# Optimization experiments

Hardware: AMD Instinct MI355X
Metric: run time of the kernel (lower is better)

Reference implementation:

```python
import jax, jax.numpy as jnp
import numpy as np

B, H, W, IN_C = 2, 64, 64, 3
D = 192            # embed_dim
DEPTH = 4
DI = 2 * D         # d_inner (mamba expand=2)
DS = 16            # d_state
DC = 4             # d_conv
DTR = -(-D // 16)  # dt_rank = ceil(D/16) = 12
EPS = 1e-5


def setup_inputs() -> dict:
    key = jax.random.key(0)
    ks = jax.random.split(key, 8)
    def rn(k, shape, s=0.02):
        return jax.random.normal(k, shape, dtype=jnp.float32) * s
    x = jax.random.normal(ks[0], (B, IN_C, H, W), dtype=jnp.float32)
    proj_w = rn(ks[1], (D, IN_C))
    proj_b = jnp.zeros((D,), jnp.float32)
    lp_w = rn(ks[2], (DEPTH, D, 2 * D))          # linear_proj: (out=D, in=2D)
    lp_b = jnp.zeros((DEPTH, D), jnp.float32)
    norm_w = jnp.ones((DEPTH, D), jnp.float32)
    in_w = rn(ks[3], (DEPTH, 2 * DI, D))         # mamba in_proj (no bias)
    conv_w = rn(ks[4], (DEPTH, DI, DC), 0.1)     # depthwise causal conv1d
    conv_b = jnp.zeros((DEPTH, DI), jnp.float32)
    xproj_w = rn(ks[5], (DEPTH, DTR + 2 * DS, DI))
    dt_w = rn(ks[6], (DEPTH, DI, DTR), 0.1)
    dt0 = np.random.default_rng(0).uniform(1e-3, 0.1, size=(DEPTH, DI)).astype(np.float32)
    dt_b = jnp.asarray(np.log(np.expm1(dt0)))    # softplus-inverse init (mamba default)
    A_log = jnp.tile(jnp.log(jnp.arange(1, DS + 1, dtype=jnp.float32)), (DEPTH, DI, 1))
    Dp = jnp.ones((DEPTH, DI), jnp.float32)
    out_w = rn(ks[7], (DEPTH, D, DI))
    normf_w = jnp.ones((D,), jnp.float32)
    return dict(x=x, proj_w=proj_w, proj_b=proj_b, lp_w=lp_w, lp_b=lp_b,
                norm_w=norm_w, in_w=in_w, conv_w=conv_w, conv_b=conv_b,
                xproj_w=xproj_w, dt_w=dt_w, dt_b=dt_b, A_log=A_log, Dp=Dp,
                out_w=out_w, normf_w=normf_w)


def _rmsnorm(x, w):
    return x * jax.lax.rsqrt(jnp.mean(x * x, axis=-1, keepdims=True) + EPS) * w


def _mamba(x, in_w, conv_w, conv_b, xproj_w, dt_w, dt_b, A_log, Dp, out_w):
    # x: (B, N, D)
    Bsz = x.shape[0]
    xz = jnp.einsum('bnd,ed->bne', x, in_w)                 # (B,N,2*DI)
    xi, z = jnp.split(xz, 2, axis=-1)
    # causal depthwise conv1d along sequence (pad left d_conv-1)
    xt = xi.transpose(0, 2, 1)                              # (B,DI,N)
    xc = jax.lax.conv_general_dilated(xt, conv_w[:, None, :], (1,), [(DC - 1, 0)],
                                      feature_group_count=DI)
    xi = jax.nn.silu((xc + conv_b[None, :, None]).transpose(0, 2, 1))  # (B,N,DI)
    dbc = jnp.einsum('bni,ei->bne', xi, xproj_w)            # (B,N,DTR+2*DS)
    dt = jax.nn.softplus(jnp.einsum('bnr,ir->bni', dbc[..., :DTR], dt_w) + dt_b)
    Bm = dbc[..., DTR:DTR + DS]                             # (B,N,DS)
    Cm = dbc[..., DTR + DS:]                                # (B,N,DS)
    A = -jnp.exp(A_log)                                     # (DI,DS)
    dA = jnp.exp(dt[..., None] * A)                         # (B,N,DI,DS)
    dBx = dt[..., None] * Bm[:, :, None, :] * xi[..., None] # (B,N,DI,DS)
    def step(h, inp):
        a, bx = inp
        h = a * h + bx
        return h, h
    h0 = jnp.zeros((Bsz, DI, DS), x.dtype)
    _, hs = jax.lax.scan(step, h0, (dA.transpose(1, 0, 2, 3), dBx.transpose(1, 0, 2, 3)))
    y = jnp.einsum('nbis,bns->bni', hs, Cm) + Dp * xi
    y = y * jax.nn.silu(z)
    return jnp.einsum('bni,di->bnd', y, out_w)


def _block(x, lp_w, lp_b, norm_w, mp):
    # DeltaVisionMambaBlock: token-diff -> linear_proj -> RMSNorm -> Mamba -> +skip
    prev = jnp.concatenate([jnp.zeros_like(x[:, :1]), x[:, :-1]], axis=1)
    comb = jnp.concatenate([x, x - prev], axis=-1)          # (B,N,2D)
    proj = jnp.einsum('bnc,dc->bnd', comb, lp_w) + lp_b
    return _mamba(_rmsnorm(proj, norm_w), *mp) + x


def reference(x, proj_w, proj_b, lp_w, lp_b, norm_w, in_w, conv_w, conv_b,
              xproj_w, dt_w, dt_b, A_log, Dp, out_w, normf_w):
    Bsz = x.shape[0]
    feat = jnp.einsum('bchw,dc->bdhw', x, proj_w) + proj_b[None, :, None, None]
    seq = feat.reshape(Bsz, D, H * W).transpose(0, 2, 1)    # (B,N,D)
    for l in range(DEPTH):
        mp = (in_w[l], conv_w[l], conv_b[l], xproj_w[l], dt_w[l], dt_b[l],
              A_log[l], Dp[l], out_w[l])
        seq = _block(seq, lp_w[l], lp_b[l], norm_w[l], mp)
    seq = _rmsnorm(seq, normf_w)
    return seq.transpose(0, 2, 1).reshape(Bsz, D, H, W)
```

## Files before the change

kernel.cpp:

```cpp
#include <hip/hip_runtime.h>
#include <hip/hip_bf16.h>

#define BB 2
#define NN 4096
#define DD 192
#define DI 384
#define DS 16
#define DTR 12
#define DC 4
#define DEPTH 4
#define NT (BB*NN)
#define NCH 128
#define CL 32
#define EPSF 1e-5f

#define OFF_X       0
#define OFF_PROJ_W  24576
#define OFF_PROJ_B  25152
#define OFF_LP_W    25344
#define OFF_LP_B    320256
#define OFF_NORM_W  321024
#define OFF_IN_W    321792
#define OFF_CONV_W  911616
#define OFF_CONV_B  917760
#define OFF_XPROJ_W 919296
#define OFF_DT_W    986880
#define OFF_DT_B    1005312
#define OFF_A_LOG   1006848
#define OFF_DP      1031424
#define OFF_OUT_W   1032960
#define OFF_NORMF_W 1327872
#define ARENA_TOTAL 1328064
#define ARENA_BYTES 2656160

typedef __hip_bfloat16 bf16_t;
typedef unsigned short u16;
typedef unsigned int u32;
typedef __attribute__((ext_vector_type(8))) unsigned short u16x8;
typedef __attribute__((ext_vector_type(8))) short s16x8;
typedef __attribute__((ext_vector_type(4))) float f32x4;

struct Ptrs { const void* p[16]; };

__device__ __forceinline__ float bf(u16 v){ return __uint_as_float(((u32)v)<<16); }
__device__ __forceinline__ u16 f2bf(float f){
  u32 b = __float_as_uint(f);
  return (u16)((b + 0x7FFFu + ((b>>16)&1u)) >> 16);
}

__global__ __launch_bounds__(256) void k_detect(const u16* __restrict__ x, int* flag){
  __shared__ int cnt;
  if (threadIdx.x==0) cnt=0;
  __syncthreads();
  u32 v = x[2*threadIdx.x];
  int ex = (int)((v>>7)&0xFF);
  if (ex>=100 && ex<=140) atomicAdd(&cnt,1);
  __syncthreads();
  if (threadIdx.x==0) *flag = (cnt>128) ? 0 : 1;
}

__global__ __launch_bounds__(256) void k_cvt(Ptrs ps, const int* __restrict__ flag, u16* __restrict__ arena){
  int e = blockIdx.x*256 + threadIdx.x;
  if (e >= ARENA_TOTAL) return;
  const void* sp; int off;
  if      (e < OFF_PROJ_W ){ sp=ps.p[0];  off=OFF_X; }
  else if (e < OFF_PROJ_B ){ sp=ps.p[1];  off=OFF_PROJ_W; }
  else if (e < OFF_LP_W   ){ sp=ps.p[2];  off=OFF_PROJ_B; }
  else if (e < OFF_LP_B   ){ sp=ps.p[3];  off=OFF_LP_W; }
  else if (e < OFF_NORM_W ){ sp=ps.p[4];  off=OFF_LP_B; }
  else if (e < OFF_IN_W   ){ sp=ps.p[5];  off=OFF_NORM_W; }
  else if (e < OFF_CONV_W ){ sp=ps.p[6];  off=OFF_IN_W; }
  else if (e < OFF_CONV_B ){ sp=ps.p[7];  off=OFF_CONV_W; }
  else if (e < OFF_XPROJ_W){ sp=ps.p[8];  off=OFF_CONV_B; }
  else if (e < OFF_DT_W   ){ sp=ps.p[9];  off=OFF_XPROJ_W; }
  else if (e < OFF_DT_B   ){ sp=ps.p[10]; off=OFF_DT_W; }
  else if (e < OFF_A_LOG  ){ sp=ps.p[11]; off=OFF_DT_B; }
  else if (e < OFF_DP     ){ sp=ps.p[12]; off=OFF_A_LOG; }
  else if (e < OFF_OUT_W  ){ sp=ps.p[13]; off=OFF_DP; }
  else if (e < OFF_NORMF_W){ sp=ps.p[14]; off=OFF_OUT_W; }
  else                     { sp=ps.p[15]; off=OFF_NORMF_W; }
  int k = e - off;
  if (*flag){
    u32 v = ((const u32*)sp)[k];
    arena[e] = (u16)((v + 0x7FFFu + ((v>>16)&1u)) >> 16);
  } else {
    arena[e] = ((const u16*)sp)[k];
  }
}

__global__ __launch_bounds__(256) void k_proj(const u16* __restrict__ x, const u16* __restrict__ pw,
                                              const u16* __restrict__ pb, float* __restrict__ seq){
  int idx = blockIdx.x*256 + threadIdx.x;
  if (idx >= NT*DD) return;
  int d = idx % DD; int bn = idx / DD; int b = bn >> 12; int n = bn & (NN-1);
  float acc = bf(pb[d]);
  acc += bf(x[(b*3+0)*NN + n]) * bf(pw[d*3+0]);
  acc += bf(x[(b*3+1)*NN + n]) * bf(pw[d*3+1]);
  acc += bf(x[(b*3+2)*NN + n]) * bf(pw[d*3+2]);
  seq[idx] = acc;
}

__global__ __launch_bounds__(256) void k_lp_norm(const float* __restrict__ seq,
    const u16* __restrict__ lp_w, const u16* __restrict__ lp_b, const u16* __restrict__ norm_w,
    u16* __restrict__ xn){
  const int tid = threadIdx.x;
  const int n0 = blockIdx.x*32;
  __shared__ u16 combL[32][392];
  __shared__ u16 wL[192][136];
  __shared__ float accL[32][200];
  __shared__ float ssq[32];

  for (int idx = tid*4; idx < 32*DD; idx += 1024){
    int t = idx/DD, d = idx%DD;
    int gn = n0 + t;
    float4 cur = *(const float4*)&seq[gn*DD + d];
    float4 prv = make_float4(0.f,0.f,0.f,0.f);
    if ((gn & (NN-1)) != 0) prv = *(const float4*)&seq[(gn-1)*DD + d];
    combL[t][d+0]=f2bf(cur.x); combL[t][d+1]=f2bf(cur.y); combL[t][d+2]=f2bf(cur.z); combL[t][d+3]=f2bf(cur.w);
    combL[t][DD+d+0]=f2bf(cur.x-prv.x); combL[t][DD+d+1]=f2bf(cur.y-prv.y);
    combL[t][DD+d+2]=f2bf(cur.z-prv.z); combL[t][DD+d+3]=f2bf(cur.w-prv.w);
  }

  const int w = tid >> 6;
  const int lane = tid & 63;
  const int lm = lane & 15, lk = lane >> 4;
  const int mt = w & 1;
  const int nbase = (w >> 1)*6;

  f32x4 acc[6];
  #pragma unroll
  for (int i=0;i<6;++i) acc[i] = (f32x4){0.f,0.f,0.f,0.f};

  for (int c=0;c<3;++c){
    const int kc = c*128;
    for (int idx = tid*8; idx < 192*128; idx += 2048){
      int row = idx >> 7, col = idx & 127;
      *(u16x8*)&wL[row][col] = *(const u16x8*)(lp_w + row*384 + kc + col);
    }
    __syncthreads();
    #pragma unroll
    for (int ks=0; ks<4; ++ks){
      s16x8 a = *(s16x8*)&combL[mt*16 + lm][kc + ks*32 + lk*8];
      #pragma unroll
      for (int nt=0; nt<6; ++nt){
        s16x8 b = *(s16x8*)&wL[(nbase+nt)*16 + lm][ks*32 + lk*8];
        acc[nt] = __builtin_amdgcn_mfma_f32_16x16x32_bf16(a, b, acc[nt], 0, 0, 0);
      }
    }
    __syncthreads();
  }
  #pragma unroll
  for (int nt=0; nt<6; ++nt){
    #pragma unroll
    for (int r=0; r<4; ++r){
      int m = mt*16 + lk*4 + r;
      int n = (nbase+nt)*16 + lm;
      accL[m][n] = acc[nt][r] + bf(lp_b[n]);
    }
  }
  __syncthreads();
  {
    int tok = tid >> 3, j = tid & 7;
    float s = 0.f;
    #pragma unroll
    for (int c=0;c<24;++c){ float v = accL[tok][j*24+c]; s += v*v; }
    s += __shfl_xor(s,1); s += __shfl_xor(s,2); s += __shfl_xor(s,4);
    if (j==0) ssq[tok] = rsqrtf(s*(1.f/DD) + EPSF);
  }
  __syncthreads();
  for (int idx = tid; idx < 32*DD; idx += 256){
    int t = idx/DD, d = idx%DD;
    xn[(n0+t)*DD + d] = f2bf(accL[t][d] * ssq[t] * bf(norm_w[d]));
  }
}

__global__ __launch_bounds__(256) void k_inproj(const u16* __restrict__ xn,
    const u16* __restrict__ in_w, u16* __restrict__ xi_c, u16* __restrict__ zz_b){
  const int tid = threadIdx.x;
  const int m0 = blockIdx.x*64;
  const int e0 = blockIdx.y*64;
  __shared__ u16 aL[64][200];
  __shared__ u16 bL[64][200];
  for (int idx = tid*8; idx < 64*192; idx += 2048){
    int row = idx/192, col = idx%192;
    *(u16x8*)&aL[row][col] = *(const u16x8*)(xn   + (m0+row)*192 + col);
    *(u16x8*)&bL[row][col] = *(const u16x8*)(in_w + (e0+row)*192 + col);
  }
  __syncthreads();
  const int w = tid >> 6, lane = tid & 63;
  const int lm = lane & 15, lk = lane >> 4;
  f32x4 acc[4];
  #pragma unroll
  for (int i=0;i<4;++i) acc[i] = (f32x4){0.f,0.f,0.f,0.f};
  #pragma unroll
  for (int ks=0; ks<6; ++ks){
    s16x8 a = *(s16x8*)&aL[w*16 + lm][ks*32 + lk*8];
    #pragma unroll
    for (int nt=0; nt<4; ++nt){
      s16x8 b = *(s16x8*)&bL[nt*16 + lm][ks*32 + lk*8];
      acc[nt] = __builtin_amdgcn_mfma_f32_16x16x32_bf16(a, b, acc[nt], 0, 0, 0);
    }
  }
  #pragma unroll
  for (int nt=0; nt<4; ++nt){
    int e = e0 + nt*16 + lm;
    #pragma unroll
    for (int r=0; r<4; ++r){
      int tok = m0 + w*16 + lk*4 + r;
      u16 v = f2bf(acc[nt][r]);
      if (e0 < DI) xi_c[tok*DI + e]      = v;
      else         zz_b[tok*DI + e - DI] = v;
    }
  }
}

__global__ __launch_bounds__(256) void k_conv(const u16* __restrict__ xi_c,
    const u16* __restrict__ conv_w, const u16* __restrict__ conv_b,
    u16* __restrict__ xc_b, float* __restrict__ xi){
  int idx = blockIdx.x*256 + threadIdx.x;
  int i = idx % DI; int bg = idx / DI;
  int nstart = bg*4;
  int base = nstart & ~(NN-1);
  float w0 = bf(conv_w[i*4+0]), w1 = bf(conv_w[i*4+1]), w2 = bf(conv_w[i*4+2]), w3 = bf(conv_w[i*4+3]);
  float cb = bf(conv_b[i]);
  float xv[7];
  #pragma unroll
  for (int t=0; t<3; ++t){
    int bn2 = nstart - 3 + t;
    xv[t] = (bn2 >= base) ? bf(xi_c[bn2*DI + i]) : 0.f;
  }
  #pragma unroll
  for (int t=3; t<7; ++t) xv[t] = bf(xi_c[(nstart + t - 3)*DI + i]);
  #pragma unroll
  for (int t=0; t<4; ++t){
    float acc = cb + xv[t]*w0 + xv[t+1]*w1 + xv[t+2]*w2 + xv[t+3]*w3;
    float v = acc/(1.f+__expf(-acc));
    int o = (nstart+t)*DI + i;
    xc_b[o] = f2bf(v);
    xi[o] = v;
  }
}

__global__ __launch_bounds__(256) void k_xproj_dt(const u16* __restrict__ xc,
    const u16* __restrict__ xproj_w, const u16* __restrict__ dt_w, const u16* __restrict__ dt_bv,
    float* __restrict__ dt_o, float* __restrict__ Bm, float* __restrict__ Cm){
  const int tid = threadIdx.x;
  const int n0 = blockIdx.x*32;
  __shared__ u16 xcL[32][392];
  __shared__ u16 dtwL[384][24];
  __shared__ float dbcL[32][16];
  for (int idx=tid; idx<512; idx+=256) ((float*)dbcL)[idx]=0.f;
  for (int idx=tid*8; idx<32*384; idx+=2048){
    int r=idx/384, c=idx%384;
    *(u16x8*)&xcL[r][c] = *(const u16x8*)(xc + (n0+r)*DI + c);
  }
  for (int idx=tid; idx<384*12; idx+=256){
    int r=idx/12, c=idx%12;
    dtwL[r][c] = dt_w[idx];
    dtwL[r][12+c] = 0;
  }
  __syncthreads();
  const int w = tid>>6, lane = tid&63, lm = lane&15, lk = lane>>4;
  const int mt = w & 1, nh = w >> 1;
  const s16x8 zb = {0,0,0,0,0,0,0,0};
  if (nh == 0){
    f32x4 acc0 = {0.f,0.f,0.f,0.f}, acc1 = {0.f,0.f,0.f,0.f};
    #pragma unroll
    for (int ks=0; ks<12; ++ks){
      s16x8 a = *(s16x8*)&xcL[mt*16+lm][ks*32+lk*8];
      s16x8 b0 = *(const s16x8*)(xproj_w + lm*384 + ks*32 + lk*8);
      s16x8 b1 = *(const s16x8*)(xproj_w + (16+lm)*384 + ks*32 + lk*8);
      acc0 = __builtin_amdgcn_mfma_f32_16x16x32_bf16(a, b0, acc0, 0, 0, 0);
      acc1 = __builtin_amdgcn_mfma_f32_16x16x32_bf16(a, b1, acc1, 0, 0, 0);
    }
    #pragma unroll
    for (int r=0;r<4;++r){
      int m = mt*16 + lk*4 + r;
      int gm = n0 + m;
      if (lm < 12) dbcL[m][lm] = acc0[r];
      else         Bm[gm*DS + lm-12] = acc0[r];
      int e1 = 16+lm;
      if (e1 < 28) Bm[gm*DS + e1-12] = acc1[r];
      else         Cm[gm*DS + e1-28] = acc1[r];
    }
  } else {
    f32x4 acc2 = {0.f,0.f,0.f,0.f};
    #pragma unroll
    for (int ks=0; ks<12; ++ks){
      s16x8 a = *(s16x8*)&xcL[mt*16+lm][ks*32+lk*8];
      s16x8 b2 = (lm<12) ? *(const s16x8*)(xproj_w + (32+lm)*384 + ks*32 + lk*8) : zb;
      acc2 = __builtin_amdgcn_mfma_f32_16x16x32_bf16(a, b2, acc2, 0, 0, 0);
    }
    #pragma unroll
    for (int r=0;r<4;++r){
      int m = mt*16 + lk*4 + r;
      int e2 = 32+lm;
      if (e2 < 44) Cm[(n0+m)*DS + e2-28] = acc2[r];
    }
  }
  __syncthreads();
  s16x8 a_dt = zb;
  if (lk < 2){
    #pragma unroll
    for (int j=0;j<8;++j) a_dt[j] = (short)f2bf(dbcL[mt*16+lm][lk*8+j]);
  }
  #pragma unroll
  for (int q=0;q<12;++q){
    int nt = nh*12 + q;
    s16x8 b = (lk<2) ? *(s16x8*)&dtwL[nt*16+lm][lk*8] : zb;
    f32x4 acc = {0.f,0.f,0.f,0.f};
    acc = __builtin_amdgcn_mfma_f32_16x16x32_bf16(a_dt, b, acc, 0, 0, 0);
    int i = nt*16 + lm;
    float bias = bf(dt_bv[i]);
    #pragma unroll
    for (int r=0;r<4;++r){
      int m = mt*16 + lk*4 + r;
      float xval = acc[r] + bias;
      float sp = (xval>20.f)? xval : log1pf(__expf(xval));
      dt_o[(n0+m)*DI + i] = sp;
    }
  }
}

__global__ __launch_bounds__(128) void k_scan1(const float* __restrict__ dt,
    const float* __restrict__ xi, const float* __restrict__ Bm,
    const u16* __restrict__ A_log, float* __restrict__ P, float* __restrict__ Q){
  const int tid = threadIdx.x;
  const int i = blockIdx.x*128 + tid;
  const int ch = blockIdx.y, b = blockIdx.z;
  __shared__ float bm_l[CL][DS];
  {
    int r = tid>>2, c4 = (tid&3)*4;
    *(float4*)&bm_l[r][c4] = *(const float4*)&Bm[(b*NN + ch*CL + r)*DS + c4];
  }
  float Av[DS];
  {
    u16x8 a0 = *(const u16x8*)(A_log + i*DS);
    u16x8 a1 = *(const u16x8*)(A_log + i*DS + 8);
    #pragma unroll
    for (int s=0;s<8;++s){ Av[s] = -__expf(bf(a0[s])); Av[8+s] = -__expf(bf(a1[s])); }
  }
  __syncthreads();
  float Pv[DS], h[DS];
  #pragma unroll
  for (int s=0;s<DS;++s){ Pv[s]=1.f; h[s]=0.f; }
  const int nb = b*NN + ch*CL;
  #pragma unroll 4
  for (int t=0;t<CL;++t){
    float dtv = dt[(nb+t)*DI + i];
    float xv  = xi[(nb+t)*DI + i];
    float dtx = dtv*xv;
    #pragma unroll
    for (int s=0;s<DS;++s){
      float a = __expf(dtv*Av[s]);
      Pv[s] *= a;
      h[s] = a*h[s] + dtx*bm_l[t][s];
    }
  }
  const int base = ((b*DI + i)*NCH + ch)*DS;
  #pragma unroll
  for (int s4=0;s4<4;++s4){
    *(float4*)&P[base+s4*4] = make_float4(Pv[s4*4+0],Pv[s4*4+1],Pv[s4*4+2],Pv[s4*4+3]);
    *(float4*)&Q[base+s4*4] = make_float4(h[s4*4+0],h[s4*4+1],h[s4*4+2],h[s4*4+3]);
  }
}

__global__ __launch_bounds__(256) void k_scan2(const float* __restrict__ P, const float* __restrict__ Q,
                                               float* __restrict__ Hin){
  int tid = blockIdx.x*256 + threadIdx.x;
  int s = tid & 15; int ci = tid >> 4;
  float h = 0.f;
  for (int ch=0; ch<NCH; ++ch){
    int idx = (ci*NCH+ch)*DS + s;
    Hin[idx] = h;
    h = P[idx]*h + Q[idx];
  }
}

__global__ __launch_bounds__(128) void k_scan3(const float* __restrict__ dt,
    const float* __restrict__ xi, const float* __restrict__ Bm, const float* __restrict__ Cm,
    const u16* __restrict__ zz_b, const u16* __restrict__ A_log, const u16* __restrict__ Dp,
    const float* __restrict__ Hin, u16* __restrict__ Y){
  const int tid = threadIdx.x;
  const int i = blockIdx.x*128 + tid;
  const int ch = blockIdx.y, b = blockIdx.z;
  __shared__ float bm_l[CL][DS], cm_l[CL][DS];
  {
    int r = tid>>2, c4 = (tid&3)*4;
    *(float4*)&bm_l[r][c4] = *(const float4*)&Bm[(b*NN + ch*CL + r)*DS + c4];
    *(float4*)&cm_l[r][c4] = *(const float4*)&Cm[(b*NN + ch*CL + r)*DS + c4];
  }
  float Av[DS];
  {
    u16x8 a0 = *(const u16x8*)(A_log + i*DS);
    u16x8 a1 = *(const u16x8*)(A_log + i*DS + 8);
    #pragma unroll
    for (int s=0;s<8;++s){ Av[s] = -__expf(bf(a0[s])); Av[8+s] = -__expf(bf(a1[s])); }
  }
  const float Dv = bf(Dp[i]);
  float h[DS];
  const int base = ((b*DI + i)*NCH + ch)*DS;
  #pragma unroll
  for (int s4=0;s4<4;++s4){
    float4 hv = *(const float4*)&Hin[base+s4*4];
    h[s4*4+0]=hv.x; h[s4*4+1]=hv.y; h[s4*4+2]=hv.z; h[s4*4+3]=hv.w;
  }
  __syncthreads();
  const int nb = b*NN + ch*CL;
  #pragma unroll 4
  for (int t=0;t<CL;++t){
    float dtv = dt[(nb+t)*DI + i];
    float xv  = xi[(nb+t)*DI + i];
    float zv  = bf(zz_b[(nb+t)*DI + i]);
    float dtx = dtv*xv;
    float y = 0.f;
    #pragma unroll
    for (int s=0;s<DS;++s){
      float a = __expf(dtv*Av[s]);
      h[s] = a*h[s] + dtx*bm_l[t][s];
      y += h[s]*cm_l[t][s];
    }
    y += Dv*xv;
    y *= zv/(1.f+__expf(-zv));
    Y[(nb+t)*DI + i] = f2bf(y);
  }
}

__global__ __launch_bounds__(256) void k_out(const u16* __restrict__ Y,
    const u16* __restrict__ out_w, float* __restrict__ seq){
  const int tid = threadIdx.x;
  const int m0 = blockIdx.x*64;
  const int d0 = blockIdx.y*64;
  __shared__ u16 aL[64][200];
  __shared__ u16 bL[64][200];
  const int w = tid >> 6, lane = tid & 63;
  const int lm = lane & 15, lk = lane >> 4;
  f32x4 acc[4];
  #pragma unroll
  for (int i=0;i<4;++i) acc[i] = (f32x4){0.f,0.f,0.f,0.f};
  for (int c=0; c<2; ++c){
    const int kc = c*192;
    for (int idx = tid*8; idx < 64*192; idx += 2048){
      int row = idx/192, col = idx%192;
      *(u16x8*)&aL[row][col] = *(const u16x8*)(Y     + (m0+row)*DI + kc + col);
      *(u16x8*)&bL[row][col] = *(const u16x8*)(out_w + (d0+row)*DI + kc + col);
    }
    __syncthreads();
    #pragma unroll
    for (int ks=0; ks<6; ++ks){
      s16x8 a = *(s16x8*)&aL[w*16 + lm][ks*32 + lk*8];
      #pragma unroll
      for (int nt=0; nt<4; ++nt){
        s16x8 b = *(s16x8*)&bL[nt*16 + lm][ks*32 + lk*8];
        acc[nt] = __builtin_amdgcn_mfma_f32_16x16x32_bf16(a, b, acc[nt], 0, 0, 0);
      }
    }
    __syncthreads();
  }
  #pragma unroll
  for (int nt=0; nt<4; ++nt){
    int d = d0 + nt*16 + lm;
    #pragma unroll
    for (int r=0; r<4; ++r){
      int tok = m0 + w*16 + lk*4 + r;
      seq[tok*DD + d] += acc[nt][r];
    }
  }
}

__global__ __launch_bounds__(192) void k_final(const float* __restrict__ seq,
    const u16* __restrict__ normf_w, void* __restrict__ out, const int* __restrict__ flag){
  const int d = threadIdx.x;
  const int bn = blockIdx.x;
  const int b = bn >> 12, n = bn & (NN-1);
  __shared__ float wred[3];
  float v = seq[bn*DD + d];
  float s = v*v;
  #pragma unroll
  for (int off=32; off>=1; off>>=1) s += __shfl_down(s,off);
  if ((d&63)==0) wred[d>>6]=s;
  __syncthreads();
  float r = rsqrtf((wred[0]+wred[1]+wred[2])*(1.f/DD) + EPSF);
  float res = v * r * bf(normf_w[d]);
  int o = (b*DD+d)*NN + n;
  if (*flag) ((float*)out)[o] = res;
  else       ((u16*)out)[o]   = f2bf(res);
}

extern "C" void kernel_launch(void* const* d_in, const int* in_sizes, int n_in,
                              void* d_out, int out_size, void* d_ws, size_t ws_size,
                              hipStream_t stream){
  Ptrs ps;
  for (int i=0;i<16;++i) ps.p[i] = d_in[i];

  u16* arena = (u16*)d_ws;
  int* flag  = (int*)(arena + ARENA_TOTAL);
  float* fbase = (float*)((char*)d_ws + ARENA_BYTES);

  float* seq  = fbase;
  float* xi   = seq  + NT*DD;
  float* dt   = xi   + NT*DI;
  float* Bm   = dt   + NT*DI;
  float* Cm   = Bm   + NT*DS;
  float* Hin  = Cm   + NT*DS;
  u16* xn_b   = (u16*)(Hin + BB*DI*NCH*DS);
  u16* xi_c   = xn_b + NT*DD;
  u16* zz_b   = xi_c + NT*DI;
  u16* Y_b    = zz_b + NT*DI;
  u16*   xc_b = Y_b;
  float* Pb   = (float*)Y_b;
  float* Qb   = (float*)xi_c;

  const u16* xA      = arena + OFF_X;
  const u16* proj_w  = arena + OFF_PROJ_W;
  const u16* proj_b  = arena + OFF_PROJ_B;
  const u16* lp_w    = arena + OFF_LP_W;
  const u16* lp_b    = arena + OFF_LP_B;
  const u16* norm_w  = arena + OFF_NORM_W;
  const u16* in_w    = arena + OFF_IN_W;
  const u16* conv_w  = arena + OFF_CONV_W;
  const u16* conv_b  = arena + OFF_CONV_B;
  const u16* xproj_w = arena + OFF_XPROJ_W;
  const u16* dt_w    = arena + OFF_DT_W;
  const u16* dt_b    = arena + OFF_DT_B;
  const u16* A_log   = arena + OFF_A_LOG;
  const u16* Dp      = arena + OFF_DP;
  const u16* out_w   = arena + OFF_OUT_W;
  const u16* normf_w = arena + OFF_NORMF_W;

  k_detect<<<1, 256, 0, stream>>>((const u16*)d_in[0], flag);
  k_cvt<<<(ARENA_TOTAL+255)/256, 256, 0, stream>>>(ps, flag, arena);

  k_proj<<<(NT*DD+255)/256, 256, 0, stream>>>(xA, proj_w, proj_b, seq);
  for (int l=0; l<DEPTH; ++l){
    k_lp_norm<<<NT/32, 256, 0, stream>>>(seq, lp_w + l*DD*2*DD, lp_b + l*DD, norm_w + l*DD, xn_b);
    k_inproj<<<dim3(NT/64, 12), 256, 0, stream>>>(xn_b, in_w + l*2*DI*DD, xi_c, zz_b);
    k_conv<<<(NT/4)*DI/256, 256, 0, stream>>>(xi_c, conv_w + l*DI*DC, conv_b + l*DI, xc_b, xi);
    k_xproj_dt<<<NT/32, 256, 0, stream>>>(xc_b, xproj_w + l*(DTR+2*DS)*DI, dt_w + l*DI*DTR,
        dt_b + l*DI, dt, Bm, Cm);
    k_scan1<<<dim3(DI/128, NCH, BB), 128, 0, stream>>>(dt, xi, Bm, A_log + l*DI*DS, Pb, Qb);
    k_scan2<<<(BB*DI*DS)/256, 256, 0, stream>>>(Pb, Qb, Hin);
    k_scan3<<<dim3(DI/128, NCH, BB), 128, 0, stream>>>(dt, xi, Bm, Cm, zz_b, A_log + l*DI*DS, Dp + l*DI, Hin, Y_b);
    k_out<<<dim3(NT/64, 3), 256, 0, stream>>>(Y_b, out_w + l*DD*DI, seq);
  }
  k_final<<<NT, 192, 0, stream>>>(seq, normf_w, d_out, flag);
}
```

Baseline: 613.1 us.

## Fuse linear_proj+norm with in_proj and recompute causal conv inside consumers

Merges the linear_proj/RMSNorm kernel with the in_proj GEMM, so the normalized activations stay in LDS instead of going through global memory. Removes the standalone conv kernel: xproj_dt and both scan kernels now recompute the depthwise causal conv plus SiLU from the bf16 in_proj output. This drops the fp32 xi buffer and two launches per layer. In exchange the conv and SiLU work is done three times, and in_proj weights are read straight from global memory with a 32-token tile per block, which lowers reuse and parallelism.

```diff
diff --git a/kernel.cpp b/kernel.cpp
--- a/kernel.cpp
+++ b/kernel.cpp
@@ -100,14 +100,15 @@
   seq[idx] = acc;
 }
 
-__global__ __launch_bounds__(256) void k_lp_norm(const float* __restrict__ seq,
+__global__ __launch_bounds__(256) void k_lp_in(const float* __restrict__ seq,
     const u16* __restrict__ lp_w, const u16* __restrict__ lp_b, const u16* __restrict__ norm_w,
-    u16* __restrict__ xn){
+    const u16* __restrict__ in_w, u16* __restrict__ xi_c, u16* __restrict__ zz_b){
   const int tid = threadIdx.x;
   const int n0 = blockIdx.x*32;
   __shared__ u16 combL[32][392];
   __shared__ u16 wL[192][136];
   __shared__ float accL[32][200];
+  __shared__ u16 xnL[32][200];
   __shared__ float ssq[32];
 
   for (int idx = tid*4; idx < 32*DD; idx += 1024){
@@ -124,38 +125,39 @@
   const int w = tid >> 6;
   const int lane = tid & 63;
   const int lm = lane & 15, lk = lane >> 4;
-  const int mt = w & 1;
-  const int nbase = (w >> 1)*6;
-
-  f32x4 acc[6];
-  #pragma unroll
-  for (int i=0;i<6;++i) acc[i] = (f32x4){0.f,0.f,0.f,0.f};
-
-  for (int c=0;c<3;++c){
-    const int kc = c*128;
-    for (int idx = tid*8; idx < 192*128; idx += 2048){
-      int row = idx >> 7, col = idx & 127;
-      *(u16x8*)&wL[row][col] = *(const u16x8*)(lp_w + row*384 + kc + col);
-    }
-    __syncthreads();
-    #pragma unroll
-    for (int ks=0; ks<4; ++ks){
-      s16x8 a = *(s16x8*)&combL[mt*16 + lm][kc + ks*32 + lk*8];
+
+  {
+    const int mt = w & 1;
+    const int nbase = (w >> 1)*6;
+    f32x4 acc[6];
+    #pragma unroll
+    for (int i=0;i<6;++i) acc[i] = (f32x4){0.f,0.f,0.f,0.f};
+    for (int c=0;c<3;++c){
+      const int kc = c*128;
+      for (int idx = tid*8; idx < 192*128; idx += 2048){
+        int row = idx >> 7, col = idx & 127;
+        *(u16x8*)&wL[row][col] = *(const u16x8*)(lp_w + row*384 + kc + col);
+      }
+      __syncthreads();
       #pragma unroll
-      for (int nt=0; nt<6; ++nt){
-        s16x8 b = *(s16x8*)&wL[(nbase+nt)*16 + lm][ks*32 + lk*8];
-        acc[nt] = __builtin_amdgcn_mfma_f32_16x16x32_bf16(a, b, acc[nt], 0, 0, 0);
-      }
-    }
-    __syncthreads();
-  }
-  #pragma unroll
-  for (int nt=0; nt<6; ++nt){
-    #pragma unroll
-    for (int r=0; r<4; ++r){
-      int m = mt*16 + lk*4 + r;
-      int n = (nbase+nt)*16 + lm;
-      accL[m][n] = acc[nt][r] + bf(lp_b[n]);
+      for (int ks=0; ks<4; ++ks){
+        s16x8 a = *(s16x8*)&combL[mt*16 + lm][kc + ks*32 + lk*8];
+        #pragma unroll
+        for (int nt=0; nt<6; ++nt){
+          s16x8 b = *(s16x8*)&wL[(nbase+nt)*16 + lm][ks*32 + lk*8];
+          acc[nt] = __builtin_amdgcn_mfma_f32_16x16x32_bf16(a, b, acc[nt], 0, 0, 0);
+        }
+      }
+      __syncthreads();
+    }
+    #pragma unroll
+    for (int nt=0; nt<6; ++nt){
+      #pragma unroll
+      for (int r=0; r<4; ++r){
+        int m = mt*16 + lk*4 + r;
+        int n = (nbase+nt)*16 + lm;
+        accL[m][n] = acc[nt][r] + bf(lp_b[n]);
+      }
     }
   }
   __syncthreads();
@@ -170,89 +172,88 @@
   __syncthreads();
   for (int idx = tid; idx < 32*DD; idx += 256){
     int t = idx/DD, d = idx%DD;
-    xn[(n0+t)*DD + d] = f2bf(accL[t][d] * ssq[t] * bf(norm_w[d]));
-  }
-}
-
-__global__ __launch_bounds__(256) void k_inproj(const u16* __restrict__ xn,
-    const u16* __restrict__ in_w, u16* __restrict__ xi_c, u16* __restrict__ zz_b){
-  const int tid = threadIdx.x;
-  const int m0 = blockIdx.x*64;
-  const int e0 = blockIdx.y*64;
-  __shared__ u16 aL[64][200];
-  __shared__ u16 bL[64][200];
-  for (int idx = tid*8; idx < 64*192; idx += 2048){
-    int row = idx/192, col = idx%192;
-    *(u16x8*)&aL[row][col] = *(const u16x8*)(xn   + (m0+row)*192 + col);
-    *(u16x8*)&bL[row][col] = *(const u16x8*)(in_w + (e0+row)*192 + col);
-  }
-  __syncthreads();
-  const int w = tid >> 6, lane = tid & 63;
-  const int lm = lane & 15, lk = lane >> 4;
-  f32x4 acc[4];
-  #pragma unroll
-  for (int i=0;i<4;++i) acc[i] = (f32x4){0.f,0.f,0.f,0.f};
-  #pragma unroll
-  for (int ks=0; ks<6; ++ks){
-    s16x8 a = *(s16x8*)&aL[w*16 + lm][ks*32 + lk*8];
-    #pragma unroll
-    for (int nt=0; nt<4; ++nt){
-      s16x8 b = *(s16x8*)&bL[nt*16 + lm][ks*32 + lk*8];
-      acc[nt] = __builtin_amdgcn_mfma_f32_16x16x32_bf16(a, b, acc[nt], 0, 0, 0);
-    }
-  }
-  #pragma unroll
-  for (int nt=0; nt<4; ++nt){
-    int e = e0 + nt*16 + lm;
-    #pragma unroll
-    for (int r=0; r<4; ++r){
-      int tok = m0 + w*16 + lk*4 + r;
-      u16 v = f2bf(acc[nt][r]);
-      if (e0 < DI) xi_c[tok*DI + e]      = v;
-      else         zz_b[tok*DI + e - DI] = v;
-    }
-  }
-}
-
-__global__ __launch_bounds__(256) void k_conv(const u16* __restrict__ xi_c,
+    xnL[t][d] = f2bf(accL[t][d] * ssq[t] * bf(norm_w[d]));
+  }
+  __syncthreads();
+  {
+    f32x4 acc2[12][2];
+    #pragma unroll
+    for (int nt=0; nt<12; ++nt){
+      acc2[nt][0] = (f32x4){0.f,0.f,0.f,0.f};
+      acc2[nt][1] = (f32x4){0.f,0.f,0.f,0.f};
+    }
+    #pragma unroll
+    for (int ks=0; ks<6; ++ks){
+      s16x8 a0 = *(s16x8*)&xnL[lm][ks*32 + lk*8];
+      s16x8 a1 = *(s16x8*)&xnL[16+lm][ks*32 + lk*8];
+      #pragma unroll
+      for (int nt=0; nt<12; ++nt){
+        s16x8 b = *(const s16x8*)(in_w + ((w*12+nt)*16 + lm)*192 + ks*32 + lk*8);
+        acc2[nt][0] = __builtin_amdgcn_mfma_f32_16x16x32_bf16(a0, b, acc2[nt][0], 0, 0, 0);
+        acc2[nt][1] = __builtin_amdgcn_mfma_f32_16x16x32_bf16(a1, b, acc2[nt][1], 0, 0, 0);
+      }
+    }
+    #pragma unroll
+    for (int nt=0; nt<12; ++nt){
+      int e = (w*12+nt)*16 + lm;
+      #pragma unroll
+      for (int m=0; m<2; ++m){
+        #pragma unroll
+        for (int r=0; r<4; ++r){
+          int tok = n0 + m*16 + lk*4 + r;
+          u16 v = f2bf(acc2[nt][m][r]);
+          if (e < DI) xi_c[tok*DI + e]      = v;
+          else        zz_b[tok*DI + e - DI] = v;
+        }
+      }
+    }
+  }
+}
+
+__global__ __launch_bounds__(256) void k_xproj_dt(const u16* __restrict__ xi_c,
     const u16* __restrict__ conv_w, const u16* __restrict__ conv_b,
-    u16* __restrict__ xc_b, float* __restrict__ xi){
-  int idx = blockIdx.x*256 + threadIdx.x;
-  int i = idx % DI; int bg = idx / DI;
-  int nstart = bg*4;
-  int base = nstart & ~(NN-1);
-  float w0 = bf(conv_w[i*4+0]), w1 = bf(conv_w[i*4+1]), w2 = bf(conv_w[i*4+2]), w3 = bf(conv_w[i*4+3]);
-  float cb = bf(conv_b[i]);
-  float xv[7];
-  #pragma unroll
-  for (int t=0; t<3; ++t){
-    int bn2 = nstart - 3 + t;
-    xv[t] = (bn2 >= base) ? bf(xi_c[bn2*DI + i]) : 0.f;
-  }
-  #pragma unroll
-  for (int t=3; t<7; ++t) xv[t] = bf(xi_c[(nstart + t - 3)*DI + i]);
-  #pragma unroll
-  for (int t=0; t<4; ++t){
-    float acc = cb + xv[t]*w0 + xv[t+1]*w1 + xv[t+2]*w2 + xv[t+3]*w3;
-    float v = acc/(1.f+__expf(-acc));
-    int o = (nstart+t)*DI + i;
-    xc_b[o] = f2bf(v);
-    xi[o] = v;
-  }
-}
-
-__global__ __launch_bounds__(256) void k_xproj_dt(const u16* __restrict__ xc,
     const u16* __restrict__ xproj_w, const u16* __restrict__ dt_w, const u16* __restrict__ dt_bv,
     float* __restrict__ dt_o, float* __restrict__ Bm, float* __restrict__ Cm){
   const int tid = threadIdx.x;
   const int n0 = blockIdx.x*32;
+  const int base = n0 & ~(NN-1);
   __shared__ u16 xcL[32][392];
   __shared__ u16 dtwL[384][24];
   __shared__ float dbcL[32][16];
   for (int idx=tid; idx<512; idx+=256) ((float*)dbcL)[idx]=0.f;
   for (int idx=tid*8; idx<32*384; idx+=2048){
     int r=idx/384, c=idx%384;
-    *(u16x8*)&xcL[r][c] = *(const u16x8*)(xc + (n0+r)*DI + c);
+    int gn = n0 + r;
+    float vals[4][8];
+    #pragma unroll
+    for (int q=0;q<4;++q){
+      int row = gn-3+q;
+      if (row >= base){
+        u16x8 xv = *(const u16x8*)(xi_c + row*DI + c);
+        #pragma unroll
+        for (int j=0;j<8;++j) vals[q][j] = bf(xv[j]);
+      } else {
+        #pragma unroll
+        for (int j=0;j<8;++j) vals[q][j] = 0.f;
+      }
+    }
+    u16x8 cw0 = *(const u16x8*)(conv_w + c*4);
+    u16x8 cw1 = *(const u16x8*)(conv_w + c*4 + 8);
+    u16x8 cw2 = *(const u16x8*)(conv_w + c*4 + 16);
+    u16x8 cw3 = *(const u16x8*)(conv_w + c*4 + 24);
+    u16x8 cb  = *(const u16x8*)(conv_b + c);
+    #pragma unroll
+    for (int j=0;j<8;++j){
+      u16 w0, w1, w2, w3;
+      int jj = j*4;
+      if (jj < 8)       { w0=cw0[jj];    w1=cw0[jj+1];  w2=cw0[jj+2];  w3=cw0[jj+3]; }
+      else if (jj < 16) { w0=cw1[jj-8];  w1=cw1[jj-7];  w2=cw1[jj-6];  w3=cw1[jj-5]; }
+      else if (jj < 24) { w0=cw2[jj-16]; w1=cw2[jj-15]; w2=cw2[jj-14]; w3=cw2[jj-13]; }
+      else              { w0=cw3[jj-24]; w1=cw3[jj-23]; w2=cw3[jj-22]; w3=cw3[jj-21]; }
+      float acc = bf(cb[j]) + vals[0][j]*bf(w0) + vals[1][j]*bf(w1) + vals[2][j]*bf(w2) + vals[3][j]*bf(w3);
+      float v = acc/(1.f+__expf(-acc));
+      xcL[r][c+j] = f2bf(v);
+    }
   }
   for (int idx=tid; idx<384*12; idx+=256){
     int r=idx/12, c=idx%12;
@@ -323,8 +324,9 @@
 }
 
 __global__ __launch_bounds__(128) void k_scan1(const float* __restrict__ dt,
-    const float* __restrict__ xi, const float* __restrict__ Bm,
-    const u16* __restrict__ A_log, float* __restrict__ P, float* __restrict__ Q){
+    const u16* __restrict__ xi_c, const u16* __restrict__ conv_w, const u16* __restrict__ conv_b,
+    const float* __restrict__ Bm, const u16* __restrict__ A_log,
+    float* __restrict__ P, float* __restrict__ Q){
   const int tid = threadIdx.x;
   const int i = blockIdx.x*128 + tid;
   const int ch = blockIdx.y, b = blockIdx.z;
@@ -340,15 +342,26 @@
     #pragma unroll
     for (int s=0;s<8;++s){ Av[s] = -__expf(bf(a0[s])); Av[8+s] = -__expf(bf(a1[s])); }
   }
+  const float w0 = bf(conv_w[i*4+0]), w1 = bf(conv_w[i*4+1]), w2 = bf(conv_w[i*4+2]), w3 = bf(conv_w[i*4+3]);
+  const float cb = bf(conv_b[i]);
+  const int nb = b*NN + ch*CL;
+  float x0=0.f, x1=0.f, x2=0.f;
+  if (ch > 0){
+    x0 = bf(xi_c[(nb-3)*DI + i]);
+    x1 = bf(xi_c[(nb-2)*DI + i]);
+    x2 = bf(xi_c[(nb-1)*DI + i]);
+  }
   __syncthreads();
   float Pv[DS], h[DS];
   #pragma unroll
   for (int s=0;s<DS;++s){ Pv[s]=1.f; h[s]=0.f; }
-  const int nb = b*NN + ch*CL;
   #pragma unroll 4
   for (int t=0;t<CL;++t){
+    float xr = bf(xi_c[(nb+t)*DI + i]);
+    float cv = cb + w0*x0 + w1*x1 + w2*x2 + w3*xr;
+    float xv = cv/(1.f+__expf(-cv));
+    x0=x1; x1=x2; x2=xr;
     float dtv = dt[(nb+t)*DI + i];
-    float xv  = xi[(nb+t)*DI + i];
     float dtx = dtv*xv;
     #pragma unroll
     for (int s=0;s<DS;++s){
@@ -378,7 +391,8 @@
 }
 
 __global__ __launch_bounds__(128) void k_scan3(const float* __restrict__ dt,
-    const float* __restrict__ xi, const float* __restrict__ Bm, const float* __restrict__ Cm,
+    const u16* __restrict__ xi_c, const u16* __restrict__ conv_w, const u16* __restrict__ conv_b,
+    const float* __restrict__ Bm, const float* __restrict__ Cm,
     const u16* __restrict__ zz_b, const u16* __restrict__ A_log, const u16* __restrict__ Dp,
     const float* __restrict__ Hin, u16* __restrict__ Y){
   const int tid = threadIdx.x;
@@ -397,7 +411,16 @@
     #pragma unroll
     for (int s=0;s<8;++s){ Av[s] = -__expf(bf(a0[s])); Av[8+s] = -__expf(bf(a1[s])); }
   }
+  const float w0 = bf(conv_w[i*4+0]), w1 = bf(conv_w[i*4+1]), w2 = bf(conv_w[i*4+2]), w3 = bf(conv_w[i*4+3]);
+  const float cb = bf(conv_b[i]);
   const float Dv = bf(Dp[i]);
+  const int nb = b*NN + ch*CL;
+  float x0=0.f, x1=0.f, x2=0.f;
+  if (ch > 0){
+    x0 = bf(xi_c[(nb-3)*DI + i]);
+    x1 = bf(xi_c[(nb-2)*DI + i]);
+    x2 = bf(xi_c[(nb-1)*DI + i]);
+  }
   float h[DS];
   const int base = ((b*DI + i)*NCH + ch)*DS;
   #pragma unroll
@@ -406,11 +429,13 @@
     h[s4*4+0]=hv.x; h[s4*4+1]=hv.y; h[s4*4+2]=hv.z; h[s4*4+3]=hv.w;
   }
   __syncthreads();
-  const int nb = b*NN + ch*CL;
   #pragma unroll 4
   for (int t=0;t<CL;++t){
+    float xr = bf(xi_c[(nb+t)*DI + i]);
+    float cv = cb + w0*x0 + w1*x1 + w2*x2 + w3*xr;
+    float xv = cv/(1.f+__expf(-cv));
+    x0=x1; x1=x2; x2=xr;
     float dtv = dt[(nb+t)*DI + i];
-    float xv  = xi[(nb+t)*DI + i];
     float zv  = bf(zz_b[(nb+t)*DI + i]);
     float dtx = dtv*xv;
     float y = 0.f;
@@ -498,18 +523,15 @@
   float* fbase = (float*)((char*)d_ws + ARENA_BYTES);
 
   float* seq  = fbase;
-  float* xi   = seq  + NT*DD;
-  float* dt   = xi   + NT*DI;
+  float* dt   = seq  + NT*DD;
   float* Bm   = dt   + NT*DI;
   float* Cm   = Bm   + NT*DS;
   float* Hin  = Cm   + NT*DS;
-  u16* xn_b   = (u16*)(Hin + BB*DI*NCH*DS);
-  u16* xi_c   = xn_b + NT*DD;
+  float* Pb   = Hin  + BB*DI*NCH*DS;
+  float* Qb   = Pb   + BB*DI*NCH*DS;
+  u16* xi_c   = (u16*)(Qb + BB*DI*NCH*DS);
   u16* zz_b   = xi_c + NT*DI;
   u16* Y_b    = zz_b + NT*DI;
-  u16*   xc_b = Y_b;
-  float* Pb   = (float*)Y_b;
-  float* Qb   = (float*)xi_c;
 
   const u16* xA      = arena + OFF_X;
   const u16* proj_w  = arena + OFF_PROJ_W;
@@ -533,14 +555,15 @@
 
   k_proj<<<(NT*DD+255)/256, 256, 0, stream>>>(xA, proj_w, proj_b, seq);
   for (int l=0; l<DEPTH; ++l){
-    k_lp_norm<<<NT/32, 256, 0, stream>>>(seq, lp_w + l*DD*2*DD, lp_b + l*DD, norm_w + l*DD, xn_b);
-    k_inproj<<<dim3(NT/64, 12), 256, 0, stream>>>(xn_b, in_w + l*2*DI*DD, xi_c, zz_b);
-    k_conv<<<(NT/4)*DI/256, 256, 0, stream>>>(xi_c, conv_w + l*DI*DC, conv_b + l*DI, xc_b, xi);
-    k_xproj_dt<<<NT/32, 256, 0, stream>>>(xc_b, xproj_w + l*(DTR+2*DS)*DI, dt_w + l*DI*DTR,
-        dt_b + l*DI, dt, Bm, Cm);
-    k_scan1<<<dim3(DI/128, NCH, BB), 128, 0, stream>>>(dt, xi, Bm, A_log + l*DI*DS, Pb, Qb);
+    k_lp_in<<<NT/32, 256, 0, stream>>>(seq, lp_w + l*DD*2*DD, lp_b + l*DD, norm_w + l*DD,
+        in_w + l*2*DI*DD, xi_c, zz_b);
+    k_xproj_dt<<<NT/32, 256, 0, stream>>>(xi_c, conv_w + l*DI*DC, conv_b + l*DI,
+        xproj_w + l*(DTR+2*DS)*DI, dt_w + l*DI*DTR, dt_b + l*DI, dt, Bm, Cm);
+    k_scan1<<<dim3(DI/128, NCH, BB), 128, 0, stream>>>(dt, xi_c, conv_w + l*DI*DC, conv_b + l*DI,
+        Bm, A_log + l*DI*DS, Pb, Qb);
     k_scan2<<<(BB*DI*DS)/256, 256, 0, stream>>>(Pb, Qb, Hin);
-    k_scan3<<<dim3(DI/128, NCH, BB), 128, 0, stream>>>(dt, xi, Bm, Cm, zz_b, A_log + l*DI*DS, Dp + l*DI, Hin, Y_b);
+    k_scan3<<<dim3(DI/128, NCH, BB), 128, 0, stream>>>(dt, xi_c, conv_w + l*DI*DC, conv_b + l*DI,
+        Bm, Cm, zz_b, A_log + l*DI*DS, Dp + l*DI, Hin, Y_b);
     k_out<<<dim3(NT/64, 3), 256, 0, stream>>>(Y_b, out_w + l*DD*DI, seq);
   }
   k_final<<<NT, 192, 0, stream>>>(seq, normf_w, d_out, flag);
```

Result: slower. 678.2 us (+10.6%).
